# Performance work log

Measured on AMD Instinct MI355X. Metric: run time of the kernel, lower is better.

## Reference

```python
import jax, jax.numpy as jnp
import numpy as np

B = 2
H_GRID, W_GRID, RADIUS = 48, 48, 3
D_MODEL, N_HEADS, D_HEAD = 512, 8, 64
N = H_GRID * W_GRID          # 2304 tokens
WSIZE = (2 * RADIUS + 1) ** 2  # 49 neighbors per token
D_ACT = D_HEAD                # d_head even -> d_act = d_head
SCALE = D_ACT ** -0.5
NEG = -1e9


def _grid_neighbors():
    rr = np.arange(N) // W_GRID
    cc = np.arange(N) % W_GRID
    off = np.arange(-RADIUS, RADIUS + 1)
    dr, dc = np.meshgrid(off, off, indexing='ij')
    dr, dc = dr.ravel(), dc.ravel()
    nr = rr[:, None] + dr[None, :]
    nc = cc[:, None] + dc[None, :]
    valid = (nr >= 0) & (nr < H_GRID) & (nc >= 0) & (nc < W_GRID)
    idx = np.clip(nr, 0, H_GRID - 1) * W_GRID + np.clip(nc, 0, W_GRID - 1)
    pos = np.stack([rr, cc], axis=-1).astype(np.float32)
    return idx.astype(np.int32), valid, pos


def setup_inputs() -> dict:
    key = jax.random.key(0)
    ks = jax.random.split(key, 8)
    idx, valid, pos = _grid_neighbors()
    s = D_MODEL ** -0.5
    return {
        'x': jax.random.normal(ks[0], (B, N, D_MODEL), jnp.float32),
        'positions': jnp.asarray(pos),
        'W_Q': jax.random.normal(ks[1], (D_MODEL, N_HEADS * D_HEAD), jnp.float32) * s,
        'W_K': jax.random.normal(ks[2], (D_MODEL, N_HEADS * D_HEAD), jnp.float32) * s,
        'W_V': jax.random.normal(ks[3], (D_MODEL, N_HEADS * D_HEAD), jnp.float32) * s,
        'W_O': jax.random.normal(ks[4], (N_HEADS * D_HEAD, D_MODEL), jnp.float32) * s,
        # learnable active-subspace basis per head (near-identity init, QR'd in fwd)
        'U': jnp.eye(D_HEAD, D_ACT)[None] + 0.05 * jax.random.normal(ks[5], (N_HEADS, D_HEAD, D_ACT), jnp.float32),
        # per-head rotation generator frequencies: theta = dr . freqs per 2x2 block
        'freqs': 0.5 * jax.random.normal(ks[6], (N_HEADS, 2, D_HEAD // 2), jnp.float32),
        'neighbor_index': jnp.asarray(idx),
        'neighbor_mask': jnp.asarray(valid),
    }


def reference(x, positions, W_Q, W_K, W_V, W_O, U, freqs, neighbor_index, neighbor_mask):
    Bt, Nt, _ = x.shape

    def heads(h):  # (B,N,H*d) -> (B,H,N,d)
        return h.reshape(Bt, Nt, N_HEADS, D_HEAD).transpose(0, 2, 1, 3)

    Q = heads(x @ W_Q)
    K = heads(x @ W_K)
    V = heads(x @ W_V)

    # Active subspace projection Pi_act = U_ortho U_ortho^T, applied as x@U@U^T
    U_ortho = jnp.linalg.qr(U)[0]                       # (H, d, d_act)
    Q = jnp.einsum('bhnd,hde,hfe->bhnf', Q, U_ortho, U_ortho)
    K = jnp.einsum('bhnd,hde,hfe->bhnf', K, U_ortho, U_ortho)

    # per-(i,j) relative rotation: block-diagonal 2x2 rotations with
    # angles theta[h,n,w,p] = (r_j - r_i) . freqs[h,:,p]
    drel = positions[neighbor_index] - positions[:, None, :]   # (N,W,2)
    theta = jnp.einsum('nwc,hcp->hnwp', drel, freqs)           # (H,N,W,d/2)
    cos, sin = jnp.cos(theta), jnp.sin(theta)

    K_loc = K[:, :, neighbor_index]                            # (B,H,N,W,d) gather
    Ke, Ko = K_loc[..., 0::2], K_loc[..., 1::2]
    Kr_e = cos[None] * Ke - sin[None] * Ko
    Kr_o = sin[None] * Ke + cos[None] * Ko
    K_rot = jnp.stack([Kr_e, Kr_o], axis=-1).reshape(K_loc.shape)

    scores = jnp.einsum('bhnd,bhnwd->bhnw', Q, K_rot) * SCALE
    scores = jnp.where(neighbor_mask[None, None], scores, NEG)
    w = jax.nn.softmax(scores, axis=-1)

    V_loc = V[:, :, neighbor_index]                            # (B,H,N,W,d)
    out = jnp.einsum('bhnw,bhnwd->bhnd', w, V_loc)
    out = out.transpose(0, 2, 1, 3).reshape(Bt, Nt, N_HEADS * D_HEAD)
    return out @ W_O
```

## Files before the change

### kernel.cpp

```cpp
#include <hip/hip_runtime.h>
#include <math.h>


#define BB 2
#define HGRID 48
#define WGRID 48
#define NNODE (HGRID*WGRID)
#define RAD 3
#define WSZ 49
#define DMODEL 512
#define NHEAD 8
#define SCALE 0.125f
#define MROWS (BB*NNODE)
#define TPAD 141

typedef _Float16 f16;
typedef __attribute__((ext_vector_type(8))) _Float16 f16x8;
typedef __attribute__((ext_vector_type(2))) _Float16 h2;
typedef __attribute__((ext_vector_type(4))) float f32x4;

typedef union { f16x8 v8; h2 h[4]; } pack8;

#if __has_builtin(__builtin_amdgcn_fdot2)
__device__ __forceinline__ float fdot2(h2 a, h2 b, float c) {
    return __builtin_amdgcn_fdot2(a, b, c, false);
}
#else
__device__ __forceinline__ float fdot2(h2 a, h2 b, float c) {
    return fmaf((float)a.x, (float)b.x, fmaf((float)a.y, (float)b.y, c));
}
#endif

__global__ void convert_all(const float* __restrict__ x,
                            const float* __restrict__ WQ, const float* __restrict__ WK,
                            const float* __restrict__ WV, const float* __restrict__ WO,
                            f16* __restrict__ x2, f16* __restrict__ Wall) {
    int id = blockIdx.x * 256 + threadIdx.x;
    if (id < MROWS * 64) {
        int r = id >> 6, c8 = (id & 63) << 3;
        float4 a = *(const float4*)&x[(size_t)r * 512 + c8];
        float4 b = *(const float4*)&x[(size_t)r * 512 + c8 + 4];
        f16 o[8] = {(f16)a.x, (f16)a.y, (f16)a.z, (f16)a.w,
                    (f16)b.x, (f16)b.y, (f16)b.z, (f16)b.w};
        *(f16x8*)&x2[(size_t)r * 512 + c8] = *(f16x8*)o;
        return;
    }
    id -= MROWS * 64;
    if (id >= 2048 * 64) return;
    const int kb = ((id >> 6) & 63) << 3;
    const int np = (id & 63) + ((id >> 12) << 6);
    const float* S;
    int n;
    if (np < 1536) { int t = np >> 9; n = np & 511; S = (t == 0) ? WQ : (t == 1) ? WK : WV; }
    else           { n = np - 1536;  S = WO; }
    f16 o[8];
#pragma unroll
    for (int i = 0; i < 8; ++i) o[i] = (f16)S[(size_t)(kb + i) * 512 + n];
    *(f16x8*)&Wall[(size_t)np * 512 + kb] = *(f16x8*)o;
}

template<int MODE>
__global__ __launch_bounds__(256)
void mgemm(const f16* __restrict__ A, const f16* __restrict__ Bt,
           f16* __restrict__ Qh, f16* __restrict__ Kh, f16* __restrict__ Vh,
           float* __restrict__ Cf, const float* __restrict__ freqs) {
    __shared__ f16 As[128 * 64];
    __shared__ f16 Bs[128 * 64];

    const int tid = threadIdx.x;
    const int l = tid & 63, wid = tid >> 6;

    const int nbx = (MODE == 0) ? 12 : 4;
    const int cpx = (MODE == 0) ? 54 : 18;
    const int bid = blockIdx.x;
    const int swz = (bid & 7) * cpx + (bid >> 3);
    const int m0 = (swz / nbx) * 128;
    const int n0 = (swz % nbx) * 128;

    const int wm = (wid >> 1) * 64, wn = (wid & 1) * 64;
    const int fr = l & 15, fk = l >> 4;
    const int srow = l >> 3, slot = l & 7;

    f32x4 acc[4][4];
#pragma unroll
    for (int m = 0; m < 4; ++m)
#pragma unroll
        for (int n = 0; n < 4; ++n) acc[m][n] = (f32x4){0.f, 0.f, 0.f, 0.f};

    for (int kt = 0; kt < 8; ++kt) {
        const int k0 = kt * 64;
#pragma unroll
        for (int j = 0; j < 4; ++j) {
            const int r = wid * 32 + j * 8 + srow;
            const int cA = (slot ^ (r & 7)) * 8;
            const f16* gA = A + (size_t)(m0 + r) * 512 + k0 + cA;
            __builtin_amdgcn_global_load_lds(
                (const __attribute__((address_space(1))) unsigned int*)gA,
                (__attribute__((address_space(3))) unsigned int*)(As + wid * 2048 + j * 512),
                16, 0, 0);
            const f16* gB = Bt + (size_t)(n0 + r) * 512 + k0 + cA;
            __builtin_amdgcn_global_load_lds(
                (const __attribute__((address_space(1))) unsigned int*)gB,
                (__attribute__((address_space(3))) unsigned int*)(Bs + wid * 2048 + j * 512),
                16, 0, 0);
        }
        asm volatile("s_waitcnt vmcnt(0)" ::: "memory");
        __syncthreads();

        f16x8 af[4][2], bfr[4][2];
#pragma unroll
        for (int m = 0; m < 4; ++m) {
            const int row = wm + m * 16 + fr;
#pragma unroll
            for (int kk = 0; kk < 2; ++kk) {
                const int b = (kk * 64 + fk * 16) ^ ((row & 7) << 4);
                af[m][kk] = *(const f16x8*)((const char*)As + row * 128 + b);
            }
        }
#pragma unroll
        for (int n = 0; n < 4; ++n) {
            const int row = wn + n * 16 + fr;
#pragma unroll
            for (int kk = 0; kk < 2; ++kk) {
                const int b = (kk * 64 + fk * 16) ^ ((row & 7) << 4);
                bfr[n][kk] = *(const f16x8*)((const char*)Bs + row * 128 + b);
            }
        }
#pragma unroll
        for (int kk = 0; kk < 2; ++kk)
#pragma unroll
            for (int m = 0; m < 4; ++m)
#pragma unroll
                for (int n = 0; n < 4; ++n)
                    acc[m][n] = __builtin_amdgcn_mfma_f32_16x16x32_f16(
                        af[m][kk], bfr[n][kk], acc[m][n], 0, 0, 0);
        __syncthreads();
    }

    if (MODE == 0) {
#pragma unroll
        for (int nf = 0; nf < 4; ++nf) {
            const int ccol = n0 + wn + nf * 16 + fr;
            const int t = ccol >> 9;
            const int h = (ccol >> 6) & 7;
            const int d = ccol & 63;
            const int p = d >> 1;
            f16* Cp = (t == 0) ? Qh : (t == 1) ? Kh : Vh;
            const float fR = freqs[h * 64 + p];
            const float fC = freqs[h * 64 + 32 + p];
            const float sgn = (d & 1) ? 1.0f : -1.0f;
#pragma unroll
            for (int mf = 0; mf < 4; ++mf) {
#pragma unroll
                for (int i = 0; i < 4; ++i) {
                    const int grow = m0 + wm + mf * 16 + fk * 4 + i;
                    const int b_ = grow >= NNODE;
                    const int nn = grow - b_ * NNODE;
                    float val = acc[mf][nf][i];
                    float part = __shfl_xor(val, 1);
                    float outv = val;
                    if (t < 2) {
                        float th = (float)(nn / WGRID) * fR + (float)(nn % WGRID) * fC;
                        float sn, cs;
                        __sincosf(th, &sn, &cs);
                        outv = fmaf(sgn * part, sn, val * cs);
                    }
                    Cp[((size_t)((b_ * NHEAD + h) * NNODE + nn)) * 64 + d] = (f16)outv;
                }
            }
        }
    } else {
#pragma unroll
        for (int nf = 0; nf < 4; ++nf) {
            const int ccol = n0 + wn + nf * 16 + fr;
#pragma unroll
            for (int mf = 0; mf < 4; ++mf) {
#pragma unroll
                for (int i = 0; i < 4; ++i) {
                    const int grow = m0 + wm + mf * 16 + fk * 4 + i;
                    Cf[(size_t)grow * 512 + ccol] = acc[mf][nf][i];
                }
            }
        }
    }
}

__global__ __launch_bounds__(256, 4)
void attn7(const f16* __restrict__ Qh, const f16* __restrict__ Kh,
           const f16* __restrict__ Vh, f16* __restrict__ out2) {
    __shared__ h2 T[32 * TPAD];

    const int tid = threadIdx.x;
    const int wid = tid >> 6, lane = tid & 63;
    const int qs = lane >> 3, wg = lane & 7;

    const int bid = blockIdx.x;
    const int t  = bid % 72, bh = bid / 72;
    const int tr = t % 12,   tc = t / 12;
    const int r0 = tr * 4,   c0 = tc * 8;
    const int h  = bh & 7,   b_ = bh >> 3;

    const int lr0 = max(0, r0 - 3), lr1 = min(HGRID - 1, r0 + 6);
    const int lc0 = max(0, c0 - 3), lc1 = min(WGRID - 1, c0 + 10);
    const int NR = lr1 - lr0 + 1, NC = lc1 - lc0 + 1;

    const f16* Kb = Kh + (size_t)bh * NNODE * 64;
    const f16* Vb = Vh + (size_t)bh * NNODE * 64;

    const int rq = r0 + wid, cq = c0 + qs;
    const int nq = rq * WGRID + cq;
    const f16* qrow = Qh + ((size_t)bh * NNODE + nq) * 64;
    h2 q2[32];
#pragma unroll
    for (int j8 = 0; j8 < 8; ++j8) {
        pack8 v;
        v.v8 = *(const f16x8*)&qrow[j8 * 8];
#pragma unroll
        for (int k = 0; k < 4; ++k) q2[j8 * 4 + k] = v.h[k];
    }

    const int cnt = NR * NC * 8;

    f16x8 vpre[5];
#pragma unroll
    for (int s = 0; s < 5; ++s) {
        const int i = tid + s * 256;
        if (i < cnt) {
            const int row = i >> 3, p4 = i & 7;
            const int glr = row / NC, glc = row - glr * NC;
            const int n = (lr0 + glr) * WGRID + (lc0 + glc);
            vpre[s] = *(const f16x8*)&Vb[(size_t)n * 64 + p4 * 8];
        }
    }

    for (int i = tid; i < cnt; i += 256) {
        const int row = i >> 3, p4 = i & 7;
        const int glr = row / NC, glc = row - glr * NC;
        const int n = (lr0 + glr) * WGRID + (lc0 + glc);
        pack8 v;
        v.v8 = *(const f16x8*)&Kb[(size_t)n * 64 + p4 * 8];
#pragma unroll
        for (int j = 0; j < 4; ++j) T[(p4 * 4 + j) * TPAD + row] = v.h[j];
    }
    __syncthreads();

    float sc[7], es[7];
    float mx = -1e30f;
#pragma unroll
    for (int k = 0; k < 7; ++k) {
        const int w = wg + 8 * k;
        sc[k] = -1e30f;
        if (w < WSZ) {
            const int dr = w / 7 - RAD, dc = w % 7 - RAD;
            const int nr = rq + dr, nc = cq + dc;
            const bool valid = ((unsigned)nr < (unsigned)HGRID) &&
                               ((unsigned)nc < (unsigned)WGRID);
            const int nrl = min(max(nr, lr0), lr1) - lr0;
            const int ncl = min(max(nc, lc0), lc1) - lc0;
            const int row = nrl * NC + ncl;
            float s = 0.0f;
#pragma unroll
            for (int j = 0; j < 32; ++j) s = fdot2(q2[j], T[j * TPAD + row], s);
            sc[k] = valid ? s * SCALE : -1e9f;
            mx = fmaxf(mx, sc[k]);
        }
    }
#pragma unroll
    for (int o = 1; o < 8; o <<= 1) mx = fmaxf(mx, __shfl_xor(mx, o));
    float sum = 0.0f;
#pragma unroll
    for (int k = 0; k < 7; ++k) {
        const int w = wg + 8 * k;
        es[k] = 0.0f;
        if (w < WSZ) { es[k] = __expf(sc[k] - mx); sum += es[k]; }
    }
#pragma unroll
    for (int o = 1; o < 8; o <<= 1) sum += __shfl_xor(sum, o);
    const float inv = 1.0f / sum;
    float esn[7];
#pragma unroll
    for (int k = 0; k < 7; ++k) esn[k] = es[k] * inv;

    __syncthreads();

#pragma unroll
    for (int s = 0; s < 5; ++s) {
        const int i = tid + s * 256;
        if (i < cnt) {
            const int row = i >> 3, p4 = i & 7;
            pack8 v; v.v8 = vpre[s];
#pragma unroll
            for (int j = 0; j < 4; ++j) T[(p4 * 4 + j) * TPAD + row] = v.h[j];
        }
    }
    __syncthreads();

    const int dg = wg;
    float2 acc[4] = {{0, 0}, {0, 0}, {0, 0}, {0, 0}};
#pragma unroll
    for (int w = 0; w < WSZ; ++w) {
        const int dr = w / 7 - RAD, dc = w % 7 - RAD;
        const int nr = rq + dr, nc = cq + dc;
        const int nrl = min(max(nr, lr0), lr1) - lr0;
        const int ncl = min(max(nc, lc0), lc1) - lc0;
        const int row = nrl * NC + ncl;
        const float pw = __shfl(esn[w >> 3], (lane & 0x38) | (w & 7));
#pragma unroll
        for (int j = 0; j < 4; ++j) {
            h2 v2 = T[(dg * 4 + j) * TPAD + row];
            acc[j].x = fmaf(pw, (float)v2.x, acc[j].x);
            acc[j].y = fmaf(pw, (float)v2.y, acc[j].y);
        }
    }

    f16 o[8] = {(f16)acc[0].x, (f16)acc[0].y, (f16)acc[1].x, (f16)acc[1].y,
                (f16)acc[2].x, (f16)acc[2].y, (f16)acc[3].x, (f16)acc[3].y};
    const size_t rowb = (size_t)(b_ * NNODE + nq) * 512 + h * 64 + dg * 8;
    *(f16x8*)&out2[rowb] = *(f16x8*)o;
}

extern "C" void kernel_launch(void* const* d_in, const int* in_sizes, int n_in,
                              void* d_out, int out_size, void* d_ws, size_t ws_size,
                              hipStream_t stream) {
    const float* x     = (const float*)d_in[0];
    const float* WQ    = (const float*)d_in[2];
    const float* WK    = (const float*)d_in[3];
    const float* WV    = (const float*)d_in[4];
    const float* WO    = (const float*)d_in[5];
    const float* freqs = (const float*)d_in[7];

    const size_t HN = (size_t)16 * NNODE * 64;
    f16* Qh   = (f16*)d_ws;
    f16* Kh   = Qh + HN;
    f16* Vh   = Kh + HN;
    f16* x2   = Vh + HN;
    f16* Wall = x2 + (size_t)MROWS * 512;
    f16* Wo2  = Wall + (size_t)1536 * 512;

    convert_all<<<((MROWS + 2048) * 64 + 255) / 256, 256, 0, stream>>>(
        x, WQ, WK, WV, WO, x2, Wall);

    mgemm<0><<<432, 256, 0, stream>>>(x2, Wall, Qh, Kh, Vh, nullptr, freqs);

    attn7<<<16 * 72, 256, 0, stream>>>(Qh, Kh, Vh, x2);

    mgemm<1><<<144, 256, 0, stream>>>(x2, Wo2, nullptr, nullptr, nullptr,
                                      (float*)d_out, freqs);
}
```

Measured before the change: 60.01 us.

## Split GEMM template, shrink output-GEMM tiles, use incremental rotation in QK epilogue

The template GEMM is split into two kernels. The output projection now uses 64x128 tiles with 288 blocks instead of 144, giving better CU occupancy on the small M=4608,N=512 GEMM. The QKV epilogue computes one sincos per 4-row group and advances the angle by the column step using a rotation recurrence, replacing a per-element sincos and integer division. The recurrence adds slight rounding drift across the four steps.

```diff
diff --git a/kernel.cpp b/kernel.cpp
--- a/kernel.cpp
+++ b/kernel.cpp
@@ -59,23 +59,20 @@
     *(f16x8*)&Wall[(size_t)np * 512 + kb] = *(f16x8*)o;
 }
 
-template<int MODE>
 __global__ __launch_bounds__(256)
-void mgemm(const f16* __restrict__ A, const f16* __restrict__ Bt,
-           f16* __restrict__ Qh, f16* __restrict__ Kh, f16* __restrict__ Vh,
-           float* __restrict__ Cf, const float* __restrict__ freqs) {
+void mgemm0(const f16* __restrict__ A, const f16* __restrict__ Bt,
+            f16* __restrict__ Qh, f16* __restrict__ Kh, f16* __restrict__ Vh,
+            const float* __restrict__ freqs) {
     __shared__ f16 As[128 * 64];
     __shared__ f16 Bs[128 * 64];
 
     const int tid = threadIdx.x;
     const int l = tid & 63, wid = tid >> 6;
 
-    const int nbx = (MODE == 0) ? 12 : 4;
-    const int cpx = (MODE == 0) ? 54 : 18;
     const int bid = blockIdx.x;
-    const int swz = (bid & 7) * cpx + (bid >> 3);
-    const int m0 = (swz / nbx) * 128;
-    const int n0 = (swz % nbx) * 128;
+    const int swz = (bid & 7) * 54 + (bid >> 3);
+    const int m0 = (swz / 12) * 128;
+    const int n0 = (swz % 12) * 128;
 
     const int wm = (wid >> 1) * 64, wn = (wid & 1) * 64;
     const int fr = l & 15, fk = l >> 4;
@@ -137,18 +134,42 @@
         __syncthreads();
     }
 
-    if (MODE == 0) {
-#pragma unroll
-        for (int nf = 0; nf < 4; ++nf) {
-            const int ccol = n0 + wn + nf * 16 + fr;
-            const int t = ccol >> 9;
-            const int h = (ccol >> 6) & 7;
-            const int d = ccol & 63;
-            const int p = d >> 1;
-            f16* Cp = (t == 0) ? Qh : (t == 1) ? Kh : Vh;
+#pragma unroll
+    for (int nf = 0; nf < 4; ++nf) {
+        const int ccol = n0 + wn + nf * 16 + fr;
+        const int t = ccol >> 9;
+        const int h = (ccol >> 6) & 7;
+        const int d = ccol & 63;
+        const int p = d >> 1;
+        f16* Cp = (t == 0) ? Qh : (t == 1) ? Kh : Vh;
+        if (t < 2) {
             const float fR = freqs[h * 64 + p];
             const float fC = freqs[h * 64 + 32 + p];
             const float sgn = (d & 1) ? 1.0f : -1.0f;
+            float sF, cF;
+            __sincosf(fC, &sF, &cF);
+#pragma unroll
+            for (int mf = 0; mf < 4; ++mf) {
+                const int g0r = m0 + wm + mf * 16 + fk * 4;
+                const int b_ = g0r >= NNODE;
+                const int nn0 = g0r - b_ * NNODE;
+                const int rr = nn0 / WGRID;
+                const int cc0 = nn0 - rr * WGRID;
+                float sn, cs;
+                __sincosf((float)rr * fR + (float)cc0 * fC, &sn, &cs);
+                const size_t base = ((size_t)((b_ * NHEAD + h) * NNODE + nn0)) * 64 + d;
+#pragma unroll
+                for (int i = 0; i < 4; ++i) {
+                    float val = acc[mf][nf][i];
+                    float part = __shfl_xor(val, 1);
+                    float outv = fmaf(sgn * part, sn, val * cs);
+                    Cp[base + (size_t)i * 64] = (f16)outv;
+                    float cs2 = cs * cF - sn * sF;
+                    sn = sn * cF + cs * sF;
+                    cs = cs2;
+                }
+            }
+        } else {
 #pragma unroll
             for (int mf = 0; mf < 4; ++mf) {
 #pragma unroll
@@ -156,30 +177,102 @@
                     const int grow = m0 + wm + mf * 16 + fk * 4 + i;
                     const int b_ = grow >= NNODE;
                     const int nn = grow - b_ * NNODE;
-                    float val = acc[mf][nf][i];
-                    float part = __shfl_xor(val, 1);
-                    float outv = val;
-                    if (t < 2) {
-                        float th = (float)(nn / WGRID) * fR + (float)(nn % WGRID) * fC;
-                        float sn, cs;
-                        __sincosf(th, &sn, &cs);
-                        outv = fmaf(sgn * part, sn, val * cs);
-                    }
-                    Cp[((size_t)((b_ * NHEAD + h) * NNODE + nn)) * 64 + d] = (f16)outv;
+                    Cp[((size_t)((b_ * NHEAD + h) * NNODE + nn)) * 64 + d] =
+                        (f16)acc[mf][nf][i];
                 }
             }
         }
-    } else {
-#pragma unroll
-        for (int nf = 0; nf < 4; ++nf) {
-            const int ccol = n0 + wn + nf * 16 + fr;
-#pragma unroll
-            for (int mf = 0; mf < 4; ++mf) {
-#pragma unroll
-                for (int i = 0; i < 4; ++i) {
-                    const int grow = m0 + wm + mf * 16 + fk * 4 + i;
-                    Cf[(size_t)grow * 512 + ccol] = acc[mf][nf][i];
-                }
+    }
+}
+
+__global__ __launch_bounds__(256)
+void mgemm1(const f16* __restrict__ A, const f16* __restrict__ Bt,
+            float* __restrict__ Cf) {
+    __shared__ f16 As[64 * 64];
+    __shared__ f16 Bs[128 * 64];
+
+    const int tid = threadIdx.x;
+    const int l = tid & 63, wid = tid >> 6;
+
+    const int bid = blockIdx.x;
+    const int swz = (bid & 7) * 36 + (bid >> 3);
+    const int m0 = (swz >> 2) * 64;
+    const int n0 = (swz & 3) * 128;
+
+    const int wm = (wid >> 1) * 32, wn = (wid & 1) * 64;
+    const int fr = l & 15, fk = l >> 4;
+    const int srow = l >> 3, slot = l & 7;
+
+    f32x4 acc[2][4];
+#pragma unroll
+    for (int m = 0; m < 2; ++m)
+#pragma unroll
+        for (int n = 0; n < 4; ++n) acc[m][n] = (f32x4){0.f, 0.f, 0.f, 0.f};
+
+    for (int kt = 0; kt < 8; ++kt) {
+        const int k0 = kt * 64;
+#pragma unroll
+        for (int j = 0; j < 2; ++j) {
+            const int r = wid * 16 + j * 8 + srow;
+            const int cA = (slot ^ (r & 7)) * 8;
+            const f16* gA = A + (size_t)(m0 + r) * 512 + k0 + cA;
+            __builtin_amdgcn_global_load_lds(
+                (const __attribute__((address_space(1))) unsigned int*)gA,
+                (__attribute__((address_space(3))) unsigned int*)(As + wid * 1024 + j * 512),
+                16, 0, 0);
+        }
+#pragma unroll
+        for (int j = 0; j < 4; ++j) {
+            const int r = wid * 32 + j * 8 + srow;
+            const int cA = (slot ^ (r & 7)) * 8;
+            const f16* gB = Bt + (size_t)(n0 + r) * 512 + k0 + cA;
+            __builtin_amdgcn_global_load_lds(
+                (const __attribute__((address_space(1))) unsigned int*)gB,
+                (__attribute__((address_space(3))) unsigned int*)(Bs + wid * 2048 + j * 512),
+                16, 0, 0);
+        }
+        asm volatile("s_waitcnt vmcnt(0)" ::: "memory");
+        __syncthreads();
+
+        f16x8 af[2][2], bfr[4][2];
+#pragma unroll
+        for (int m = 0; m < 2; ++m) {
+            const int row = wm + m * 16 + fr;
+#pragma unroll
+            for (int kk = 0; kk < 2; ++kk) {
+                const int b = (kk * 64 + fk * 16) ^ ((row & 7) << 4);
+                af[m][kk] = *(const f16x8*)((const char*)As + row * 128 + b);
+            }
+        }
+#pragma unroll
+        for (int n = 0; n < 4; ++n) {
+            const int row = wn + n * 16 + fr;
+#pragma unroll
+            for (int kk = 0; kk < 2; ++kk) {
+                const int b = (kk * 64 + fk * 16) ^ ((row & 7) << 4);
+                bfr[n][kk] = *(const f16x8*)((const char*)Bs + row * 128 + b);
+            }
+        }
+#pragma unroll
+        for (int kk = 0; kk < 2; ++kk)
+#pragma unroll
+            for (int m = 0; m < 2; ++m)
+#pragma unroll
+                for (int n = 0; n < 4; ++n)
+                    acc[m][n] = __builtin_amdgcn_mfma_f32_16x16x32_f16(
+                        af[m][kk], bfr[n][kk], acc[m][n], 0, 0, 0);
+        __syncthreads();
+    }
+
+#pragma unroll
+    for (int nf = 0; nf < 4; ++nf) {
+        const int ccol = n0 + wn + nf * 16 + fr;
+#pragma unroll
+        for (int mf = 0; mf < 2; ++mf) {
+#pragma unroll
+            for (int i = 0; i < 4; ++i) {
+                const int grow = m0 + wm + mf * 16 + fk * 4 + i;
+                Cf[(size_t)grow * 512 + ccol] = acc[mf][nf][i];
             }
         }
     }
@@ -340,10 +433,9 @@
     convert_all<<<((MROWS + 2048) * 64 + 255) / 256, 256, 0, stream>>>(
         x, WQ, WK, WV, WO, x2, Wall);
 
-    mgemm<0><<<432, 256, 0, stream>>>(x2, Wall, Qh, Kh, Vh, nullptr, freqs);
+    mgemm0<<<432, 256, 0, stream>>>(x2, Wall, Qh, Kh, Vh, freqs);
 
     attn7<<<16 * 72, 256, 0, stream>>>(Qh, Kh, Vh, x2);
 
-    mgemm<1><<<144, 256, 0, stream>>>(x2, Wo2, nullptr, nullptr, nullptr,
-                                      (float*)d_out, freqs);
-}
+    mgemm1<<<288, 256, 0, stream>>>(x2, Wo2, (float*)d_out);
+}
```

Result: faster. 56.25 us (-6.3%).
